# Kernel tuning notes

Hardware: AMD Instinct MI355X
Metric: run time of the kernel (lower is better)

The kernel has to match this reference:

```python
import math
import jax, jax.numpy as jnp
import numpy as np

B, S, D = 2, 4096, 2048
H, DK, DV, SEG = 16, 128, 128, 512
DH = 8192
LN_EPS = 1e-5


def setup_inputs() -> dict:
    key = jax.random.key(0)
    ks = jax.random.split(key, 12)
    s = 0.02
    return {
        "x": jax.random.normal(ks[0], (B, S, D), dtype=jnp.float32),
        "Wq": jax.random.normal(ks[1], (D, H * DK), dtype=jnp.float32) * s,
        "Wk": jax.random.normal(ks[2], (D, H * DK), dtype=jnp.float32) * s,
        "Wv": jax.random.normal(ks[3], (D, H * DV), dtype=jnp.float32) * s,
        "Wo": jax.random.normal(ks[4], (H * DV, D), dtype=jnp.float32) * s,
        "betas": jax.random.normal(ks[5], (1, H, 1, DV), dtype=jnp.float32),
        "W1": jax.random.normal(ks[6], (D, DH), dtype=jnp.float32) * s,
        "b1": jnp.zeros((DH,), dtype=jnp.float32),
        "W2": jax.random.normal(ks[7], (DH, D), dtype=jnp.float32) * s,
        "b2": jnp.zeros((D,), dtype=jnp.float32),
        "ln_g": jnp.ones((D,), dtype=jnp.float32),
        "ln_b": jnp.zeros((D,), dtype=jnp.float32),
    }


def _split_segments(t, n_seg, hd):
    # (B, S, H*hd) -> (n_seg, B, H, SEG, hd)
    t = t.reshape(B, n_seg, SEG, H, hd)
    return jnp.transpose(t, (1, 0, 3, 2, 4))


def reference(x, Wq, Wk, Wv, Wo, betas, W1, b1, W2, b2, ln_g, ln_b):
    n_seg = S // SEG
    q = _split_segments(x @ Wq, n_seg, DK)
    k = _split_segments(x @ Wk, n_seg, DK)
    v = _split_segments(x @ Wv, n_seg, DV)

    causal_mask = jnp.tril(jnp.ones((SEG, SEG), dtype=bool))
    gate = jax.nn.sigmoid(betas)  # (1,H,1,DV)
    scale = 1.0 / math.sqrt(DK)

    def step(carry, qkv):
        mem, z = carry  # mem: (B,H,DK,DV), z: (B,H,DK,1)
        qs, ks_, vs = qkv  # (B,H,SEG,dk/dv)
        sig_q = jax.nn.elu(qs) + 1.0
        # standard SDP attention within the segment
        scores = jnp.einsum('bhsd,bhtd->bhst', qs, ks_) * scale
        scores = jnp.where(causal_mask, scores, -jnp.inf)
        att_dot = jnp.einsum('bhst,bhtv->bhsv', jax.nn.softmax(scores, axis=-1), vs)
        # memory retrieval (normalized linear attention)
        att_mem = jnp.einsum('bhsd,bhdv->bhsv', sig_q, mem) / jnp.einsum('bhsd,bhdo->bhso', sig_q, z)
        # linear memory update
        sig_k = jax.nn.elu(ks_) + 1.0
        mem = mem + jnp.einsum('bhsd,bhsv->bhdv', sig_k, vs)
        z = z + jnp.sum(sig_k, axis=2)[..., None]
        att = gate * att_mem + (1.0 - gate) * att_dot  # (B,H,SEG,DV)
        return (mem, z), att

    mem0 = jnp.zeros((B, H, DK, DV), dtype=x.dtype)
    z0 = jnp.ones((B, H, DK, 1), dtype=x.dtype) / DK
    _, outs = jax.lax.scan(step, (mem0, z0), (q, k, v))  # (n_seg,B,H,SEG,DV)

    att = jnp.transpose(outs, (1, 0, 3, 2, 4)).reshape(B, S, H * DV)
    attn_out = att @ Wo
    # MLP (dropout = 0)
    h = jax.nn.relu(attn_out @ W1 + b1)
    y = h @ W2 + b2
    # residual + LayerNorm
    res = y + x
    mu = jnp.mean(res, axis=-1, keepdims=True)
    var = jnp.var(res, axis=-1, keepdims=True)
    return (res - mu) / jnp.sqrt(var + LN_EPS) * ln_g + ln_b
```

## Files before the change

kernel.cpp:

```cpp
#include <hip/hip_runtime.h>

typedef short s16x8 __attribute__((ext_vector_type(8)));
typedef unsigned short u16x8 __attribute__((ext_vector_type(8)));
typedef unsigned short u16x4 __attribute__((ext_vector_type(4)));
typedef float f32x4 __attribute__((ext_vector_type(4)));

#define CB 2
#define CS 4096
#define CD 2048
#define CH 16
#define CSEG 512
#define CDH 8192

__device__ __forceinline__ unsigned short f2b(float f) {
  union { float f; unsigned u; } v; v.f = f;
  unsigned r = v.u + 0x7fffu + ((v.u >> 16) & 1u);
  return (unsigned short)(r >> 16);
}
__device__ __forceinline__ float b2f(unsigned short b) {
  union { unsigned u; float f; } v; v.u = ((unsigned)b) << 16;
  return v.f;
}
__device__ __forceinline__ f32x4 mfma16(s16x8 a, s16x8 b, f32x4 c) {
  return __builtin_amdgcn_mfma_f32_16x16x32_bf16(a, b, c, 0, 0, 0);
}
__device__ __forceinline__ void async16(const unsigned short* g, unsigned short* l) {
  __builtin_amdgcn_global_load_lds((const __attribute__((address_space(1))) void*)g,
                                   (__attribute__((address_space(3))) void*)l, 16, 0, 0);
}

__global__ void convert_bf16_k(const float* __restrict__ in, unsigned short* __restrict__ out) {
  size_t i = ((size_t)blockIdx.x * 256 + threadIdx.x) * 4;
  f32x4 v = *(const f32x4*)(in + i);
  u16x4 o;
  #pragma unroll
  for (int e = 0; e < 4; e++) o[e] = f2b(v[e]);
  *(u16x4*)(out + i) = o;
}

__global__ void transpose_bf16_k(const float* __restrict__ in, unsigned short* __restrict__ out,
                                 int R, int C) {
  __shared__ float tile[32][33];
  int c0 = blockIdx.x * 32, r0 = blockIdx.y * 32;
  int tx = threadIdx.x & 31, ty = threadIdx.x >> 5;
  #pragma unroll
  for (int i = 0; i < 32; i += 8)
    tile[ty + i][tx] = in[(size_t)(r0 + ty + i) * C + c0 + tx];
  __syncthreads();
  #pragma unroll
  for (int i = 0; i < 32; i += 8)
    out[(size_t)(c0 + ty + i) * R + r0 + tx] = f2b(tile[tx][ty + i]);
}

__global__ void transpose_kv_k(const unsigned short* __restrict__ kb,
                               const unsigned short* __restrict__ vb,
                               unsigned short* __restrict__ KT,
                               unsigned short* __restrict__ VT) {
  __shared__ unsigned short kt_[64][72];
  __shared__ unsigned short vt_[64][72];
  const int t = threadIdx.x;
  const int r0 = blockIdx.x * 64, c0 = blockIdx.y * 64;
  {
    int row = t >> 2, cc = (t & 3) * 16;
    size_t g = (size_t)(r0 + row) * CD + c0 + cc;
    #pragma unroll
    for (int u = 0; u < 2; u++) {
      u16x8 kv = *(const u16x8*)(kb + g + u * 8);
      u16x8 vv = *(const u16x8*)(vb + g + u * 8);
      u16x8 ko;
      #pragma unroll
      for (int e = 0; e < 8; e++) {
        float f = b2f(kv[e]);
        ko[e] = f2b(f > 0.f ? f + 1.f : __expf(f));
      }
      *(u16x8*)&kt_[row][cc + u * 8] = ko;
      *(u16x8*)&vt_[row][cc + u * 8] = vv;
    }
  }
  __syncthreads();
  {
    int vc = t >> 2, s0 = (t & 3) * 16;
    int c = c0 + vc;
    int h = c >> 7, v = c & 127;
    int b = r0 >> 12, sbase = (r0 & 4095) + s0;
    size_t obase = ((size_t)((b * 16 + h) * 128 + v) << 12) + sbase;
    u16x8 wk0, wk1, wv0, wv1;
    #pragma unroll
    for (int e = 0; e < 8; e++) {
      wk0[e] = kt_[s0 + e][vc];      wv0[e] = vt_[s0 + e][vc];
      wk1[e] = kt_[s0 + 8 + e][vc];  wv1[e] = vt_[s0 + 8 + e][vc];
    }
    *(u16x8*)&KT[obase] = wk0;  *(u16x8*)&KT[obase + 8] = wk1;
    *(u16x8*)&VT[obase] = wv0;  *(u16x8*)&VT[obase + 8] = wv1;
  }
}

template <int EPI>
__global__ __launch_bounds__(512, 2) void gemm256(const unsigned short* __restrict__ A,
                                                  const unsigned short* __restrict__ BT,
                                                  const float* __restrict__ bias,
                                                  unsigned short* __restrict__ C,
                                                  int M, int N, int K) {
  __shared__ unsigned short As[2 * 16384];
  __shared__ unsigned short Bs[2 * 16384];

  const int t = threadIdx.x, wave = t >> 6, lane = t & 63;
  const int fr = lane & 15, quad = lane >> 4;
  const int wm = wave >> 2, wn = wave & 3;
  const int wave8 = wave * 8;

  const int nwg = (int)gridDim.x;
  const int q8 = nwg >> 3;
  const int wg = (blockIdx.x & 7) * q8 + (blockIdx.x >> 3);
  const int nN = N >> 8;
  const int stripe = wg / (8 * nN), rem = wg % (8 * nN);
  const int m0 = (stripe * 8 + (rem & 7)) << 8;
  const int n0 = (rem >> 3) << 8;

  const int NT = K >> 6;

  const int scol = ((t & 7) ^ ((t >> 3) & 7)) * 8;
  const unsigned short* Asrc = A + (size_t)(m0 + (t >> 3)) * K + scol;
  const unsigned short* Bsrc = BT + (size_t)(n0 + (t >> 3)) * K + scol;

  const int sw0 = ((quad ^ (fr & 7)) * 8);
  const int sw1 = (((4 + quad) ^ (fr & 7)) * 8);
  const int arow = wm * 128 + fr;
  const int brow = wn * 64 + fr;

  f32x4 c00[4][2] = {}, c01[4][2] = {}, c11[4][2] = {}, c10[4][2] = {};
  s16x8 aC[4][2], b0f[2][2], b1f[2][2];

#define STG2(SRC, LB, HR, KT)                                                            \
  do {                                                                                   \
    async16((SRC) + (size_t)(HR) * K + (size_t)(KT) * 64, (LB) + ((HR) + wave8) * 64);   \
    async16((SRC) + (size_t)((HR) + 64) * K + (size_t)(KT) * 64,                         \
            (LB) + ((HR) + 64 + wave8) * 64);                                            \
  } while (0)

#define LDA4(DST, BASE, ROFF)                                          \
  _Pragma("unroll") for (int m_ = 0; m_ < 4; m_++) {                   \
    const unsigned short* p_ = (BASE) + (size_t)(arow + (ROFF) + m_ * 16) * 64; \
    DST[m_][0] = *(const s16x8*)(p_ + sw0);                            \
    DST[m_][1] = *(const s16x8*)(p_ + sw1);                            \
  }

#define LDB2(DST, BASE, ROFF)                                          \
  _Pragma("unroll") for (int n_ = 0; n_ < 2; n_++) {                   \
    const unsigned short* p_ = (BASE) + (size_t)(brow + (ROFF) + n_ * 16) * 64; \
    DST[n_][0] = *(const s16x8*)(p_ + sw0);                            \
    DST[n_][1] = *(const s16x8*)(p_ + sw1);                            \
  }

#define MFMA_Q(CC, AV, BV)                                             \
  _Pragma("unroll") for (int k_ = 0; k_ < 2; k_++)                     \
  _Pragma("unroll") for (int m_ = 0; m_ < 4; m_++)                     \
  _Pragma("unroll") for (int n_ = 0; n_ < 2; n_++)                     \
      CC[m_][n_] = mfma16(AV[m_][k_], BV[n_][k_], CC[m_][n_]);

  {
    unsigned short* A0 = As;           unsigned short* B0 = Bs;
    unsigned short* A1 = As + 16384;   unsigned short* B1 = Bs + 16384;
    STG2(Bsrc, B0, 0, 0);   STG2(Bsrc, B0, 128, 0);
    STG2(Asrc, A0, 0, 0);   STG2(Asrc, A0, 128, 0);
    STG2(Bsrc, B1, 0, 1);   STG2(Bsrc, B1, 128, 1);
    STG2(Asrc, A1, 0, 1);   STG2(Asrc, A1, 128, 1);
  }
  asm volatile("s_waitcnt vmcnt(8)" ::: "memory");
  __builtin_amdgcn_s_barrier();

  for (int tt = 0; tt < NT; tt++) {
    const int cur = tt & 1;
    unsigned short* Ac = As + (cur << 14);
    unsigned short* Bc = Bs + (cur << 14);
    const int k2 = (tt + 2 < NT) ? tt + 2 : NT - 1;

    LDA4(aC, Ac, 0)
    LDB2(b0f, Bc, 0)
    __builtin_amdgcn_s_barrier();
    asm volatile("s_waitcnt lgkmcnt(0)" ::: "memory");
    __builtin_amdgcn_sched_barrier(0);
    __builtin_amdgcn_s_setprio(1);
    MFMA_Q(c00, aC, b0f)
    __builtin_amdgcn_s_setprio(0);
    __builtin_amdgcn_s_barrier();

    LDB2(b1f, Bc, 32)
    __builtin_amdgcn_s_barrier();
    asm volatile("s_waitcnt lgkmcnt(0)" ::: "memory");
    __builtin_amdgcn_sched_barrier(0);
    __builtin_amdgcn_s_setprio(1);
    MFMA_Q(c01, aC, b1f)
    __builtin_amdgcn_s_setprio(0);
    __builtin_amdgcn_s_barrier();

    LDA4(aC, Ac, 64)
    STG2(Bsrc, Bc, 0, k2);
    STG2(Bsrc, Bc, 128, k2);
    __builtin_amdgcn_s_barrier();
    asm volatile("s_waitcnt lgkmcnt(0)" ::: "memory");
    __builtin_amdgcn_sched_barrier(0);
    __builtin_amdgcn_s_setprio(1);
    MFMA_Q(c11, aC, b1f)
    __builtin_amdgcn_s_setprio(0);
    __builtin_amdgcn_s_barrier();

    asm volatile("s_waitcnt vmcnt(4)" ::: "memory");
    STG2(Asrc, Ac, 0, k2);
    STG2(Asrc, Ac, 128, k2);
    __builtin_amdgcn_s_barrier();
    __builtin_amdgcn_s_setprio(1);
    MFMA_Q(c10, aC, b0f)
    __builtin_amdgcn_s_setprio(0);
    __builtin_amdgcn_s_barrier();
  }

  const int er = quad * 4;
#define EPIQ(CC, MH, NH)                                               \
  _Pragma("unroll") for (int m_ = 0; m_ < 4; m_++) {                   \
    int row_ = m0 + wm * 128 + (MH)*64 + m_ * 16 + er;                 \
    _Pragma("unroll") for (int n_ = 0; n_ < 2; n_++) {                 \
      int col_ = n0 + wn * 64 + (NH)*32 + n_ * 16 + fr;                \
      float bv_ = (EPI >= 2) ? bias[col_] : 0.f;                       \
      _Pragma("unroll") for (int r_ = 0; r_ < 4; r_++) {               \
        float v_ = CC[m_][n_][r_];                                     \
        size_t idx_ = (size_t)(row_ + r_) * N + col_;                  \
        if (EPI == 1) C[idx_] = f2b(v_);                               \
        else if (EPI == 2) { v_ += bv_; C[idx_] = f2b(v_ > 0.f ? v_ : 0.f); } \
        else { v_ += bv_; C[idx_] = f2b(v_); }                         \
      }                                                                \
    }                                                                  \
  }
  EPIQ(c00, 0, 0)
  EPIQ(c01, 0, 1)
  EPIQ(c11, 1, 1)
  EPIQ(c10, 1, 0)
#undef EPIQ
#undef MFMA_Q
#undef LDB2
#undef LDA4
#undef STG2
}

__global__ void kvsum_k(const unsigned short* __restrict__ KT, const unsigned short* __restrict__ VT,
                        float* __restrict__ memsegT, float* __restrict__ zseg) {
  __shared__ unsigned short As[128 * 32];
  __shared__ unsigned short Bs[128 * 32];
  const int seg = blockIdx.x, b = blockIdx.y, h = blockIdx.z;
  const int bh = b * 16 + h;
  const int t = threadIdx.x, wave = t >> 6, lane = t & 63;
  const int fr = lane & 15, fq = (lane >> 4) * 8;
  const int wr = (wave >> 1) * 64, wc = (wave & 1) * 64;

  f32x4 acc[4][4] = {};
  const size_t sbase = (size_t)seg * 512;
  const unsigned short* Ag = VT + ((size_t)(bh * 128 + wave * 32 + (lane >> 2)) << 12) + sbase + (lane & 3) * 8;
  const unsigned short* Bg = KT + ((size_t)(bh * 128 + wave * 32 + (lane >> 2)) << 12) + sbase + (lane & 3) * 8;
  unsigned short* Al = As + (wave * 32) * 32;
  unsigned short* Bl = Bs + (wave * 32) * 32;
  const size_t r16 = (size_t)16 << 12;

  for (int kk = 0; kk < 512; kk += 32) {
    __syncthreads();
    async16(Ag + kk, Al);
    async16(Ag + kk + r16, Al + 16 * 32);
    async16(Bg + kk, Bl);
    async16(Bg + kk + r16, Bl + 16 * 32);
    __syncthreads();
    s16x8 af[4], bfr[4];
    #pragma unroll
    for (int i = 0; i < 4; i++) af[i] = *(const s16x8*)&As[(wr + i * 16 + fr) * 32 + fq];
    #pragma unroll
    for (int j = 0; j < 4; j++) bfr[j] = *(const s16x8*)&Bs[(wc + j * 16 + fr) * 32 + fq];
    #pragma unroll
    for (int i = 0; i < 4; i++)
      #pragma unroll
      for (int j = 0; j < 4; j++)
        acc[i][j] = mfma16(af[i], bfr[j], acc[i][j]);
  }

  const size_t obase = (size_t)((seg * 2 + b) * 16 + h) * 16384;
  const int er = (lane >> 4) * 4, ec = lane & 15;
  #pragma unroll
  for (int i = 0; i < 4; i++)
    #pragma unroll
    for (int j = 0; j < 4; j++)
      #pragma unroll
      for (int r = 0; r < 4; r++)
        memsegT[obase + (size_t)(wr + i * 16 + er + r) * 128 + wc + j * 16 + ec] = acc[i][j][r];

  if (t < 128) {
    const unsigned short* zp = KT + ((size_t)(bh * 128 + t) << 12) + sbase;
    float z = 0.f;
    #pragma unroll 4
    for (int u = 0; u < 64; u++) {
      u16x8 kv = *(const u16x8*)(zp + u * 8);
      #pragma unroll
      for (int e = 0; e < 8; e++) z += b2f(kv[e]);
    }
    zseg[(size_t)((seg * 2 + b) * 16 + h) * 128 + t] = z;
  }
}

__global__ void prefix_k(const float* __restrict__ memsegT, const float* __restrict__ zseg,
                         unsigned short* __restrict__ memPT, float* __restrict__ zP) {
  const int bh = blockIdx.x, t = threadIdx.x;
  for (int e = t; e < 16384; e += 256) {
    float a = 0.f;
    #pragma unroll
    for (int s = 0; s < 8; s++) {
      size_t idx = (size_t)(s * 32 + bh) * 16384 + e;
      memPT[idx] = f2b(a);
      a += memsegT[idx];
    }
  }
  if (t < 128) {
    float a = 1.f / 128.f;
    #pragma unroll
    for (int s = 0; s < 8; s++) {
      size_t idx = (size_t)(s * 32 + bh) * 128 + t;
      zP[idx] = a;
      a += zseg[idx];
    }
  }
}

#define PD 136
#define PPS 40
__global__ void attn_k(const unsigned short* __restrict__ qb,
                       const unsigned short* __restrict__ kb,
                       const unsigned short* __restrict__ VT,
                       const unsigned short* __restrict__ memPT,
                       const float* __restrict__ zPv,
                       const float* __restrict__ betas,
                       unsigned short* __restrict__ att) {
  const int qt = blockIdx.x, seg = blockIdx.y, bh = blockIdx.z;
  const int b = bh >> 4, h = bh & 15;
  const int t = threadIdx.x, wave = t >> 6, lane = t & 63;
  const int fr = lane & 15, quad = lane >> 4, fq = quad * 8;

  __shared__ unsigned short Qs[64 * PD];
  __shared__ unsigned short SB[64 * PD];
  __shared__ unsigned short KB[32 * PD];
  __shared__ unsigned short VTs[128 * PPS];
  __shared__ float denomS[64];
  __shared__ float dpart[4][64];
  __shared__ float zPs[128];

  unsigned short* SQ = SB;
  unsigned short* Ps = SB;

  const size_t qrow0 = (size_t)b * CS + (size_t)seg * CSEG + (size_t)qt * 64;
  const size_t mbase = (size_t)(seg * 32 + bh) * 16384;
  const size_t vtbase = ((size_t)(bh * 128) << 12) + (size_t)seg * 512;

  {
    int row = t >> 2, c0 = (t & 3) * 32;
    const unsigned short* src = qb + (qrow0 + row) * (size_t)CD + (size_t)h * 128 + c0;
    #pragma unroll
    for (int u = 0; u < 4; u++) {
      u16x8 qv = *(const u16x8*)(src + u * 8);
      u16x8 qo, so;
      #pragma unroll
      for (int e = 0; e < 8; e++) {
        float f = b2f(qv[e]);
        qo[e] = f2b(f * 0.08838834764831845f);
        so[e] = f2b(f > 0.f ? f + 1.f : __expf(f));
      }
      *(u16x8*)&Qs[row * PD + c0 + u * 8] = qo;
      *(u16x8*)&SQ[row * PD + c0 + u * 8] = so;
    }
    if (t < 128) zPs[t] = zPv[(size_t)(seg * 32 + bh) * 128 + t];
  }
  __syncthreads();

  {
    int row = t & 63, part = t >> 6;
    float s = 0.f;
    #pragma unroll
    for (int i = 0; i < 32; i++) {
      int d = part * 32 + i;
      s += b2f(SQ[row * PD + d]) * zPs[d];
    }
    dpart[part][row] = s;
  }
  __syncthreads();
  if (t < 64) denomS[t] = dpart[0][t] + dpart[1][t] + dpart[2][t] + dpart[3][t];

  f32x4 om[8] = {};
  for (int qd = 0; qd < 4; qd++) {
    __syncthreads();
    {
      int row = t >> 3, c0 = (t & 7) * 16;
      const unsigned short* msrc = memPT + mbase + (size_t)(qd * 32 + row) * 128 + c0;
      *(u16x8*)&KB[row * PD + c0] = *(const u16x8*)msrc;
      *(u16x8*)&KB[row * PD + c0 + 8] = *(const u16x8*)(msrc + 8);
    }
    __syncthreads();
    #pragma unroll
    for (int jj = 0; jj < 2; jj++)
      #pragma unroll
      for (int kf = 0; kf < 4; kf++) {
        s16x8 a = *(const s16x8*)&SQ[(wave * 16 + fr) * PD + kf * 32 + fq];
        s16x8 bb = *(const s16x8*)&KB[(jj * 16 + fr) * PD + kf * 32 + fq];
        om[qd * 2 + jj] = mfma16(a, bb, om[qd * 2 + jj]);
      }
  }

  f32x4 od[8] = {};
  float mrow[4], lrow[4];
  #pragma unroll
  for (int r = 0; r < 4; r++) { mrow[r] = -1e30f; lrow[r] = 0.f; }

  const int nkt = qt * 2 + 2;
  for (int kt = 0; kt < nkt; kt++) {
    __syncthreads();
    {
      int row = t >> 3, c0 = (t & 7) * 16;
      size_t g = ((size_t)b * CS + (size_t)seg * CSEG + (size_t)kt * 32 + row) * CD + (size_t)h * 128 + c0;
      *(u16x8*)&KB[row * PD + c0] = *(const u16x8*)(kb + g);
      *(u16x8*)&KB[row * PD + c0 + 8] = *(const u16x8*)(kb + g + 8);
      int v = t >> 1, sc = (t & 1) * 16;
      const unsigned short* vsrc = VT + vtbase + ((size_t)v << 12) + kt * 32 + sc;
      *(u16x8*)&VTs[v * PPS + sc] = *(const u16x8*)vsrc;
      *(u16x8*)&VTs[v * PPS + sc + 8] = *(const u16x8*)(vsrc + 8);
    }
    __syncthreads();

    f32x4 sc[2] = {};
    #pragma unroll
    for (int kf = 0; kf < 4; kf++) {
      s16x8 a = *(const s16x8*)&Qs[(wave * 16 + fr) * PD + kf * 32 + fq];
      #pragma unroll
      for (int nt = 0; nt < 2; nt++) {
        s16x8 bb = *(const s16x8*)&KB[(nt * 16 + fr) * PD + kf * 32 + fq];
        sc[nt] = mfma16(a, bb, sc[nt]);
      }
    }

    if (kt >= 2 * qt) {
      #pragma unroll
      for (int nt = 0; nt < 2; nt++)
        #pragma unroll
        for (int r = 0; r < 4; r++) {
          int qi = qt * 64 + wave * 16 + quad * 4 + r;
          int ki = kt * 32 + nt * 16 + fr;
          if (ki > qi) sc[nt][r] = -1e30f;
        }
    }

    float al[4], pv[2][4];
    #pragma unroll
    for (int r = 0; r < 4; r++) {
      float mx = fmaxf(sc[0][r], sc[1][r]);
      #pragma unroll
      for (int xm = 8; xm >= 1; xm >>= 1) mx = fmaxf(mx, __shfl_xor(mx, xm, 64));
      float mn = fmaxf(mrow[r], mx);
      al[r] = __expf(mrow[r] - mn);
      mrow[r] = mn;
      float ps = 0.f;
      #pragma unroll
      for (int nt = 0; nt < 2; nt++) {
        float p = __expf(sc[nt][r] - mn);
        pv[nt][r] = p;
        ps += p;
      }
      #pragma unroll
      for (int xm = 8; xm >= 1; xm >>= 1) ps += __shfl_xor(ps, xm, 64);
      lrow[r] = lrow[r] * al[r] + ps;
    }
    #pragma unroll
    for (int j = 0; j < 8; j++)
      #pragma unroll
      for (int r = 0; r < 4; r++) od[j][r] *= al[r];

    #pragma unroll
    for (int nt = 0; nt < 2; nt++)
      #pragma unroll
      for (int r = 0; r < 4; r++)
        Ps[(wave * 16 + quad * 4 + r) * PPS + nt * 16 + fr] = f2b(pv[nt][r]);

    s16x8 a = *(const s16x8*)&Ps[(wave * 16 + fr) * PPS + fq];
    #pragma unroll
    for (int j = 0; j < 8; j++) {
      s16x8 bb = *(const s16x8*)&VTs[(j * 16 + fr) * PPS + fq];
      od[j] = mfma16(a, bb, od[j]);
    }
  }

  #pragma unroll
  for (int j = 0; j < 8; j++) {
    int vcol = j * 16 + fr;
    float g = 1.f / (1.f + __expf(-betas[h * 128 + vcol]));
    #pragma unroll
    for (int r = 0; r < 4; r++) {
      int rowl = wave * 16 + quad * 4 + r;
      float amem = om[j][r] / denomS[rowl];
      float adot = od[j][r] / lrow[r];
      att[(qrow0 + rowl) * (size_t)CD + (size_t)h * 128 + vcol] = f2b(g * amem + (1.f - g) * adot);
    }
  }
}

__global__ void ln_k(const unsigned short* __restrict__ y, const float* __restrict__ x,
                     const float* __restrict__ gam, const float* __restrict__ bet,
                     float* __restrict__ out) {
  const int row = blockIdx.x, t = threadIdx.x;
  const int lane = t & 63, wave = t >> 6;
  const unsigned short* yr = y + (size_t)row * CD;
  const float* xr = x + (size_t)row * CD;
  float v[8];
  float s = 0.f, ss = 0.f;
  u16x8 a8 = *(const u16x8*)(yr + t * 8);
  #pragma unroll
  for (int u = 0; u < 2; u++) {
    f32x4 c = *(const f32x4*)(xr + t * 8 + u * 4);
    #pragma unroll
    for (int e = 0; e < 4; e++) {
      float r = b2f(a8[u * 4 + e]) + c[e];
      v[u * 4 + e] = r; s += r; ss += r * r;
    }
  }
  #pragma unroll
  for (int off = 32; off >= 1; off >>= 1) {
    s += __shfl_xor(s, off, 64);
    ss += __shfl_xor(ss, off, 64);
  }
  __shared__ float red[8];
  if (lane == 0) { red[wave] = s; red[4 + wave] = ss; }
  __syncthreads();
  s = red[0] + red[1] + red[2] + red[3];
  ss = red[4] + red[5] + red[6] + red[7];
  const float mu = s * (1.f / 2048.f);
  const float var = ss * (1.f / 2048.f) - mu * mu;
  const float rs = rsqrtf(var + 1e-5f);
  #pragma unroll
  for (int u = 0; u < 2; u++)
    #pragma unroll
    for (int e = 0; e < 4; e++) {
      int c = t * 8 + u * 4 + e;
      out[(size_t)row * CD + c] = (v[u * 4 + e] - mu) * rs * gam[c] + bet[c];
    }
}

extern "C" void kernel_launch(void* const* d_in, const int* in_sizes, int n_in,
                              void* d_out, int out_size, void* d_ws, size_t ws_size,
                              hipStream_t stream) {
  const float* xf   = (const float*)d_in[0];
  const float* Wq   = (const float*)d_in[1];
  const float* Wk   = (const float*)d_in[2];
  const float* Wv   = (const float*)d_in[3];
  const float* Wo   = (const float*)d_in[4];
  const float* bet  = (const float*)d_in[5];
  const float* W1   = (const float*)d_in[6];
  const float* b1   = (const float*)d_in[7];
  const float* W2   = (const float*)d_in[8];
  const float* b2   = (const float*)d_in[9];
  const float* lng  = (const float*)d_in[10];
  const float* lnb  = (const float*)d_in[11];
  float* out = (float*)d_out;

  const size_t MB = 1024ull * 1024ull;
  char* w = (char*)d_ws;
  unsigned short* qbuf  = (unsigned short*)(w + 0 * MB);
  unsigned short* kbuf  = (unsigned short*)(w + 32 * MB);
  unsigned short* vbuf  = (unsigned short*)(w + 64 * MB);
  unsigned short* xb    = (unsigned short*)(w + 96 * MB);
  unsigned short* VTg   = (unsigned short*)(w + 96 * MB);
  unsigned short* KTg   = (unsigned short*)(w + 128 * MB);
  unsigned short* attb  = (unsigned short*)(w + 128 * MB);
  float*          msegT = (float*)(w + 64 * MB);
  unsigned short* memPT = (unsigned short*)(w + 80 * MB);
  float*          zsegb = (float*)(w + 88 * MB);
  float*          zPb   = (float*)(w + 89 * MB);
  unsigned short* aob   = (unsigned short*)(w + 0 * MB);
  unsigned short* hb    = (unsigned short*)(w + 32 * MB);
  unsigned short* ybb   = (unsigned short*)(w + 0 * MB);
  unsigned short* W1T   = (unsigned short*)(w + 160 * MB);
  unsigned short* W2T   = (unsigned short*)(w + 160 * MB);
  unsigned short* WqT   = (unsigned short*)(w + 192 * MB);
  unsigned short* WkT   = (unsigned short*)(w + 200 * MB);
  unsigned short* WvT   = (unsigned short*)(w + 208 * MB);
  unsigned short* WoT   = (unsigned short*)(w + 216 * MB);

  convert_bf16_k<<<dim3(16384), 256, 0, stream>>>(xf, xb);
  transpose_bf16_k<<<dim3(64, 64), 256, 0, stream>>>(Wq, WqT, 2048, 2048);
  transpose_bf16_k<<<dim3(64, 64), 256, 0, stream>>>(Wk, WkT, 2048, 2048);
  transpose_bf16_k<<<dim3(64, 64), 256, 0, stream>>>(Wv, WvT, 2048, 2048);
  transpose_bf16_k<<<dim3(64, 64), 256, 0, stream>>>(Wo, WoT, 2048, 2048);
  transpose_bf16_k<<<dim3(256, 64), 256, 0, stream>>>(W1, W1T, 2048, 8192);

  gemm256<1><<<dim3(256), 512, 0, stream>>>(xb, WqT, nullptr, qbuf, 8192, 2048, 2048);
  gemm256<1><<<dim3(256), 512, 0, stream>>>(xb, WkT, nullptr, kbuf, 8192, 2048, 2048);
  gemm256<1><<<dim3(256), 512, 0, stream>>>(xb, WvT, nullptr, vbuf, 8192, 2048, 2048);

  transpose_kv_k<<<dim3(128, 32), 256, 0, stream>>>(kbuf, vbuf, KTg, VTg);
  kvsum_k<<<dim3(8, 2, 16), 256, 0, stream>>>(KTg, VTg, msegT, zsegb);
  prefix_k<<<dim3(32), 256, 0, stream>>>(msegT, zsegb, memPT, zPb);
  attn_k<<<dim3(8, 8, 32), 256, 0, stream>>>(qbuf, kbuf, VTg, memPT, zPb, bet, attb);

  gemm256<1><<<dim3(256), 512, 0, stream>>>(attb, WoT, nullptr, aob, 8192, 2048, 2048);
  gemm256<2><<<dim3(1024), 512, 0, stream>>>(aob, W1T, b1, hb, 8192, 8192, 2048);
  transpose_bf16_k<<<dim3(64, 256), 256, 0, stream>>>(W2, W2T, 8192, 2048);
  gemm256<4><<<dim3(256), 512, 0, stream>>>(hb, W2T, b2, ybb, 8192, 2048, 8192);
  ln_k<<<dim3(8192), 256, 0, stream>>>(ybb, xf, lng, lnb, out);
}
```

Baseline: 1.281 ms.

## Replace ping-pong GEMM pipeline with simple double-buffered prefetch loop

Drops the finely interleaved four-phase schedule (barriers, setprio, sched_barrier, prefetch two tiles ahead with partial vmcnt waits). The new loop issues the global-to-LDS copy for tile tt+1 into the other buffer at the start, runs all MFMAs on the current tile, then waits for all loads and takes one barrier. This cuts barrier count and simplifies the scheduling. It loses the two-tile lookahead and the per-phase priority control, so memory latency may be exposed more and wave ping-pong overlap is lost.

Measured after the change: 1.283 ms. Within noise of the previous version (+0.2%).

```diff
diff --git a/kernel.cpp b/kernel.cpp
--- a/kernel.cpp
+++ b/kernel.cpp
@@ -158,61 +158,36 @@
   _Pragma("unroll") for (int n_ = 0; n_ < 2; n_++)                     \
       CC[m_][n_] = mfma16(AV[m_][k_], BV[n_][k_], CC[m_][n_]);
 
-  {
-    unsigned short* A0 = As;           unsigned short* B0 = Bs;
-    unsigned short* A1 = As + 16384;   unsigned short* B1 = Bs + 16384;
-    STG2(Bsrc, B0, 0, 0);   STG2(Bsrc, B0, 128, 0);
-    STG2(Asrc, A0, 0, 0);   STG2(Asrc, A0, 128, 0);
-    STG2(Bsrc, B1, 0, 1);   STG2(Bsrc, B1, 128, 1);
-    STG2(Asrc, A1, 0, 1);   STG2(Asrc, A1, 128, 1);
-  }
-  asm volatile("s_waitcnt vmcnt(8)" ::: "memory");
+  STG2(Bsrc, Bs, 0, 0);  STG2(Bsrc, Bs, 128, 0);
+  STG2(Asrc, As, 0, 0);  STG2(Asrc, As, 128, 0);
+  asm volatile("s_waitcnt vmcnt(0)" ::: "memory");
   __builtin_amdgcn_s_barrier();
+  asm volatile("" ::: "memory");
 
   for (int tt = 0; tt < NT; tt++) {
     const int cur = tt & 1;
     unsigned short* Ac = As + (cur << 14);
     unsigned short* Bc = Bs + (cur << 14);
-    const int k2 = (tt + 2 < NT) ? tt + 2 : NT - 1;
+
+    if (tt + 1 < NT) {
+      unsigned short* An = As + ((cur ^ 1) << 14);
+      unsigned short* Bn = Bs + ((cur ^ 1) << 14);
+      STG2(Bsrc, Bn, 0, tt + 1);  STG2(Bsrc, Bn, 128, tt + 1);
+      STG2(Asrc, An, 0, tt + 1);  STG2(Asrc, An, 128, tt + 1);
+    }
 
     LDA4(aC, Ac, 0)
     LDB2(b0f, Bc, 0)
+    MFMA_Q(c00, aC, b0f)
+    LDB2(b1f, Bc, 32)
+    MFMA_Q(c01, aC, b1f)
+    LDA4(aC, Ac, 64)
+    MFMA_Q(c11, aC, b1f)
+    MFMA_Q(c10, aC, b0f)
+
+    asm volatile("s_waitcnt vmcnt(0)" ::: "memory");
     __builtin_amdgcn_s_barrier();
-    asm volatile("s_waitcnt lgkmcnt(0)" ::: "memory");
-    __builtin_amdgcn_sched_barrier(0);
-    __builtin_amdgcn_s_setprio(1);
-    MFMA_Q(c00, aC, b0f)
-    __builtin_amdgcn_s_setprio(0);
-    __builtin_amdgcn_s_barrier();
-
-    LDB2(b1f, Bc, 32)
-    __builtin_amdgcn_s_barrier();
-    asm volatile("s_waitcnt lgkmcnt(0)" ::: "memory");
-    __builtin_amdgcn_sched_barrier(0);
-    __builtin_amdgcn_s_setprio(1);
-    MFMA_Q(c01, aC, b1f)
-    __builtin_amdgcn_s_setprio(0);
-    __builtin_amdgcn_s_barrier();
-
-    LDA4(aC, Ac, 64)
-    STG2(Bsrc, Bc, 0, k2);
-    STG2(Bsrc, Bc, 128, k2);
-    __builtin_amdgcn_s_barrier();
-    asm volatile("s_waitcnt lgkmcnt(0)" ::: "memory");
-    __builtin_amdgcn_sched_barrier(0);
-    __builtin_amdgcn_s_setprio(1);
-    MFMA_Q(c11, aC, b1f)
-    __builtin_amdgcn_s_setprio(0);
-    __builtin_amdgcn_s_barrier();
-
-    asm volatile("s_waitcnt vmcnt(4)" ::: "memory");
-    STG2(Asrc, Ac, 0, k2);
-    STG2(Asrc, Ac, 128, k2);
-    __builtin_amdgcn_s_barrier();
-    __builtin_amdgcn_s_setprio(1);
-    MFMA_Q(c10, aC, b0f)
-    __builtin_amdgcn_s_setprio(0);
-    __builtin_amdgcn_s_barrier();
+    asm volatile("" ::: "memory");
   }
 
   const int er = quad * 4;
```
